# Kernel tuning notes

Measured on AMD Instinct MI355X. Metric: run time of the kernel, lower is better.

## Reference

```python
import jax, jax.numpy as jnp
import numpy as np
from jax import lax

B, H, W, CL, CC, CD, NH, NP = 8, 48, 48, 384, 384, 384, 12, 4
N = H * W
HD = CL // NH
SCALE = HD ** -0.5


def _pool_mat(n, out=7):
    # torch AdaptiveAvgPool2d bin edges: [floor(i*n/out), ceil((i+1)*n/out))
    M = np.zeros((out, n), np.float32)
    for i in range(out):
        s = (i * n) // out
        e = -(-((i + 1) * n) // out)
        M[i, s:e] = 1.0 / (e - s)
    return jnp.asarray(M)


def _resize_mat(out_n, in_n):
    # bilinear, align_corners=False (torch F.interpolate)
    M = np.zeros((out_n, in_n), np.float32)
    scale = in_n / out_n
    for o in range(out_n):
        src = (o + 0.5) * scale - 0.5
        src = min(max(src, 0.0), in_n - 1.0)
        i0 = int(np.floor(src))
        i1 = min(i0 + 1, in_n - 1)
        f = src - i0
        M[o, i0] += 1.0 - f
        M[o, i1] += f
    return jnp.asarray(M)


def _ln_c(x, g, b):
    # LayerNorm over channel dim of NCHW, eps=1e-6
    mu = jnp.mean(x, axis=1, keepdims=True)
    var = jnp.mean((x - mu) ** 2, axis=1, keepdims=True)
    xn = (x - mu) * lax.rsqrt(var + 1e-6)
    return xn * g[None, :, None, None] + b[None, :, None, None]


def _c1(x, w):
    # 1x1 conv, w: (out,in)
    return jnp.einsum('oc,bchw->bohw', w, x)


def _bilerp(feat, grid):
    # feat (G,C,Hs,Ws), grid (G,M,2) xy in [-1,1]; align_corners=False, zero padding
    G, C, Hs, Ws = feat.shape
    x = (grid[..., 0] + 1.0) * 0.5 * Ws - 0.5
    y = (grid[..., 1] + 1.0) * 0.5 * Hs - 0.5
    x0 = jnp.floor(x)
    y0 = jnp.floor(y)
    fx = x - x0
    fy = y - y0
    featf = feat.transpose(0, 2, 3, 1).reshape(G, Hs * Ws, C)
    x0i = x0.astype(jnp.int32)
    y0i = y0.astype(jnp.int32)

    def corner(ix, iy):
        valid = ((ix >= 0) & (ix < Ws) & (iy >= 0) & (iy < Hs)).astype(feat.dtype)
        flat = jnp.clip(iy, 0, Hs - 1) * Ws + jnp.clip(ix, 0, Ws - 1)
        g = jax.vmap(lambda f, i: f[i])(featf, flat)  # (G,M,C)
        return g * valid[..., None]

    v00 = corner(x0i, y0i)
    v01 = corner(x0i + 1, y0i)
    v10 = corner(x0i, y0i + 1)
    v11 = corner(x0i + 1, y0i + 1)
    w00 = ((1 - fx) * (1 - fy))[..., None]
    w01 = (fx * (1 - fy))[..., None]
    w10 = ((1 - fx) * fy)[..., None]
    w11 = (fx * fy)[..., None]
    return v00 * w00 + v01 * w01 + v10 * w10 + v11 * w11  # (G,M,C)


def _forward(local_feat, context_prior, deformable_x, W_q, W_k, W_v, W_pre, ln1_g, ln1_b,
             W_post, dw_w, dw_b, ln2_g, ln2_b, W_lo, b_lo, W_off, b_off,
             attention_biases, W_p, bn_g, bn_b, bn_mean, bn_var):
    q = _c1(local_feat, W_q)  # (B,CL,H,W)

    # context_offset_guide: 1x1 -> GELU -> adaptive pool 7x7 -> LN(C) -> 1x1 to 32 -> resize
    cg = jax.nn.gelu(_c1(context_prior, W_pre), approximate=False)
    Mh, Mw = _pool_mat(H), _pool_mat(W)
    pooled = jnp.einsum('oh,pw,bchw->bcop', Mh, Mw, cg)
    guide = _c1(_ln_c(pooled, ln1_g, ln1_b), W_post)  # (B,32,7,7)
    Uh, Uw = _resize_mat(H, 7), _resize_mat(W, 7)
    guide = jnp.einsum('Oh,Pw,bchw->bcOP', Uh, Uw, guide)  # (B,32,H,W)

    # local_offset_base: dwconv3x3 -> LN(C) -> GELU -> 1x1 to 32
    dw = lax.conv_general_dilated(local_feat, dw_w, (1, 1), [(1, 1), (1, 1)],
                                  dimension_numbers=('NCHW', 'OIHW', 'NCHW'),
                                  feature_group_count=CL) + dw_b[None, :, None, None]
    lo = jax.nn.gelu(_ln_c(dw, ln2_g, ln2_b), approximate=False)
    lo = _c1(lo, W_lo) + b_lo[None, :, None, None]  # (B,32,H,W)

    fused = jnp.concatenate([guide, lo], axis=1)  # (B,64,H,W)
    off = _c1(fused, W_off) + b_off[None, :, None, None]  # (B,NH*NP*2,H,W)
    off = off.transpose(0, 2, 3, 1).reshape(B, H, W, NH, NP, 2)
    offn = off / jnp.asarray([W, H], dtype=off.dtype)

    ry = (jnp.arange(H, dtype=off.dtype) + 0.5) / H
    rx = (jnp.arange(W, dtype=off.dtype) + 0.5) / W
    ref = jnp.stack([jnp.broadcast_to(rx[None, :], (H, W)),
                     jnp.broadcast_to(ry[:, None], (H, W))], axis=-1)  # (H,W,2) xy
    grid = (ref[None, :, :, None, None, :] + offn) * 2.0 - 1.0  # (B,H,W,NH,NP,2)

    gridh = grid.reshape(B, N, NH, NP, 2).transpose(0, 2, 1, 3, 4)  # (B,NH,N,NP,2)
    grid_r = gridh.reshape(B * NH, N * NP, 2)

    k = _c1(context_prior, W_k).reshape(B * NH, HD, H, W)
    v = _c1(deformable_x, W_v).reshape(B * NH, HD, H, W)
    k_s = _bilerp(k, grid_r).reshape(B, NH, N, NP, HD)
    v_s = _bilerp(v, grid_r).reshape(B, NH, N, NP, HD)

    qh = q.reshape(B, NH, HD, N).transpose(0, 1, 3, 2)  # (B,NH,N,HD)
    scores = jnp.einsum('bhnd,bhnpd->bhnp', qh, k_s) * SCALE

    # relative position bias: idx(p1,p2) = |dy|*W + |dx| (first-seen enumeration)
    px = jnp.clip(jnp.round((gridh[..., 0] + 1.0) * 0.5 * W - 0.5), 0, W - 1).astype(jnp.int32)
    py = jnp.clip(jnp.round((gridh[..., 1] + 1.0) * 0.5 * H - 0.5), 0, H - 1).astype(jnp.int32)
    n = jnp.arange(N, dtype=jnp.int32)
    qy = (n // W)[None, None, :, None]
    qx = (n % W)[None, None, :, None]
    bidx = jnp.abs(qy - py) * W + jnp.abs(qx - px)  # (B,NH,N,NP)
    bias = attention_biases[jnp.arange(NH)[None, :, None, None], bidx]

    attn = jax.nn.softmax(scores + bias, axis=-1)
    out = jnp.einsum('bhnp,bhnpd->bhnd', attn, v_s)  # (B,NH,N,HD)
    out = out.transpose(0, 1, 3, 2).reshape(B, CL, H, W)

    y = _c1(out, W_p)
    y = bn_g[None, :, None, None] * (y - bn_mean[None, :, None, None]) * \
        lax.rsqrt(bn_var[None, :, None, None] + 1e-5) + bn_b[None, :, None, None]
    return y


def setup_inputs():
    ks = jax.random.split(jax.random.key(0), 16)
    f32 = jnp.float32
    d = {
        'local_feat': jax.random.normal(ks[0], (B, CL, H, W), f32),
        'context_prior': jax.random.normal(ks[1], (B, CC, H, W), f32),
        'deformable_x': jax.random.normal(ks[2], (B, CD, H, W), f32),
        'W_q': jax.random.normal(ks[3], (CL, CL), f32) * 0.02,
        'W_k': jax.random.normal(ks[4], (CL, CC), f32) * 0.02,
        'W_v': jax.random.normal(ks[5], (CD, CD), f32) * 0.02,
        'W_pre': jax.random.normal(ks[6], (CC, CC), f32) * 0.02,
        'ln1_g': jnp.ones((CC,), f32),
        'ln1_b': jnp.zeros((CC,), f32),
        'W_post': jax.random.normal(ks[7], (32, CC), f32) * 0.02,
        'dw_w': jax.random.normal(ks[8], (CL, 1, 3, 3), f32) * 0.1,
        'dw_b': jnp.zeros((CL,), f32),
        'ln2_g': jnp.ones((CL,), f32),
        'ln2_b': jnp.zeros((CL,), f32),
        'W_lo': jax.random.normal(ks[9], (32, CL), f32) * 0.02,
        'b_lo': jnp.zeros((32,), f32),
        'W_off': jax.random.normal(ks[10], (NH * NP * 2, 64), f32) * 0.01,
        'b_off': jax.random.normal(ks[11], (NH * NP * 2,), f32) * 0.5,
        'attention_biases': jax.random.normal(ks[12], (NH, H * W), f32) * 0.02,
        'W_p': jax.random.normal(ks[13], (CL, CL), f32) * 0.02,
        'bn_g': jnp.ones((CL,), f32),
        'bn_b': jnp.zeros((CL,), f32),
        'bn_mean': jax.random.normal(ks[14], (CL,), f32) * 0.01,
        'bn_var': jax.random.uniform(ks[15], (CL,), f32, 0.5, 1.5),
    }
    return d


def reference(local_feat, context_prior, deformable_x, W_q, W_k, W_v, W_pre, ln1_g, ln1_b,
              W_post, dw_w, dw_b, ln2_g, ln2_b, W_lo, b_lo, W_off, b_off,
              attention_biases, W_p, bn_g, bn_b, bn_mean, bn_var):
    return _forward(local_feat, context_prior, deformable_x, W_q, W_k, W_v, W_pre, ln1_g,
                    ln1_b, W_post, dw_w, dw_b, ln2_g, ln2_b, W_lo, b_lo, W_off, b_off,
                    attention_biases, W_p, bn_g, bn_b, bn_mean, bn_var)
```

## Files before the change

### kernel.cpp

```cpp
#include <hip/hip_runtime.h>
#include <hip/hip_bf16.h>
#include <math.h>

#define B_ 8
#define H_ 48
#define W_ 48
#define N_ 2304
#define C_ 384
#define NH_ 12
#define NP_ 4
#define HD_ 32
#define SCALE_ 0.17677669529663687f

typedef unsigned short ushort;
typedef short bf16x8 __attribute__((ext_vector_type(8)));
typedef float f32x4 __attribute__((ext_vector_type(4)));

__device__ __forceinline__ float b2f(ushort u) {
    union { float f; unsigned i; } x; x.i = ((unsigned)u) << 16; return x.f;
}
__device__ __forceinline__ ushort f2b(float f) {
    __hip_bfloat16 h = __float2bfloat16(f);
    return *(ushort*)&h;
}
__device__ __forceinline__ float geluf(float x) {
    return 0.5f * x * (1.0f + erff(x * 0.70710678118654752440f));
}
__device__ __forceinline__ int iabs(int x) { return x < 0 ? -x : x; }

__device__ __forceinline__ void gl_lds16(const ushort* g, ushort* l) {
    __builtin_amdgcn_global_load_lds(
        (const __attribute__((address_space(1))) unsigned int*)g,
        (__attribute__((address_space(3))) unsigned int*)l, 16, 0, 0);
}

__global__ void probe_kernel(const void* ones_ptr, int* flag) {
    if (threadIdx.x == 0 && blockIdx.x == 0)
        *flag = (*(const unsigned*)ones_ptr == 0x3F803F80u) ? 1 : 0;
}

#define PREP_MAX 24
struct PrepTab {
    const void* src[PREP_MAX];
    void*       dst[PREP_MAX];
    int         n[PREP_MAX];
    int         tobf[PREP_MAX];
};
__global__ __launch_bounds__(256) void prep_kernel(PrepTab tab, int ne, const int* __restrict__ dflag)
{
    const int isbf = *dflag;
    const int e = blockIdx.y;
    if (e >= ne) return;
    const int n = tab.n[e];
    const void* src = tab.src[e];
    if (tab.tobf[e]) {
        ushort* dst = (ushort*)tab.dst[e];
        if (isbf) {
            const ushort* s = (const ushort*)src;
            for (int i = blockIdx.x * 256 + threadIdx.x; i < n; i += gridDim.x * 256)
                dst[i] = s[i];
        } else {
            const float* s = (const float*)src;
            for (int i = blockIdx.x * 256 + threadIdx.x; i < n; i += gridDim.x * 256)
                dst[i] = f2b(s[i]);
        }
    } else {
        float* dst = (float*)tab.dst[e];
        if (isbf) {
            const ushort* s = (const ushort*)src;
            for (int i = blockIdx.x * 256 + threadIdx.x; i < n; i += gridDim.x * 256)
                dst[i] = b2f(s[i]);
        } else {
            const float* s = (const float*)src;
            for (int i = blockIdx.x * 256 + threadIdx.x; i < n; i += gridDim.x * 256)
                dst[i] = s[i];
        }
    }
}

__global__ void dwt_prep_kernel(const float* __restrict__ WdF, float* __restrict__ WdT)
{
    int c = threadIdx.x;
#pragma unroll
    for (int u = 0; u < 9; u++) WdT[u * C_ + c] = WdF[c * 9 + u];
}

struct TPtrs { const void* src[3]; ushort* dst[3]; };
__global__ __launch_bounds__(256) void transpose3_kernel(TPtrs tp, const int* __restrict__ dflag)
{
    const int isbf = *dflag;
    const int which = blockIdx.z >> 3;
    const int b = blockIdx.z & 7;
    const int n0 = blockIdx.x * 64, c0 = blockIdx.y * 32;
    const void* in = tp.src[which];
    ushort* out = tp.dst[which];
    const int t = threadIdx.x;

    __shared__ unsigned tile[64][33];

    if (isbf) {
        {
            const int c = t >> 3, s = t & 7;
            uint4 v = *(const uint4*)((const ushort*)in + ((size_t)b * C_ + c0 + c) * N_ + n0 + s * 8);
            const int nb = s * 8;
            tile[nb + 0][c] = v.x & 0xffff; tile[nb + 1][c] = v.x >> 16;
            tile[nb + 2][c] = v.y & 0xffff; tile[nb + 3][c] = v.y >> 16;
            tile[nb + 4][c] = v.z & 0xffff; tile[nb + 5][c] = v.z >> 16;
            tile[nb + 6][c] = v.w & 0xffff; tile[nb + 7][c] = v.w >> 16;
        }
        __syncthreads();
        {
            const int n = t >> 2, s = t & 3;
            const int cb = s * 8;
            unsigned p0 = tile[n][cb + 0] | (tile[n][cb + 1] << 16);
            unsigned p1 = tile[n][cb + 2] | (tile[n][cb + 3] << 16);
            unsigned p2 = tile[n][cb + 4] | (tile[n][cb + 5] << 16);
            unsigned p3 = tile[n][cb + 6] | (tile[n][cb + 7] << 16);
            uint4 o; o.x = p0; o.y = p1; o.z = p2; o.w = p3;
            *(uint4*)(out + ((size_t)b * N_ + n0 + n) * C_ + c0 + cb) = o;
        }
    } else {
        float* tf = (float*)&tile[0][0];
        const int tx = t & 31, ty = t >> 5;
        for (int sub = 0; sub < 2; sub++) {
            int ns = n0 + sub * 32;
            __syncthreads();
#pragma unroll
            for (int u = 0; u < 4; u++) {
                int c = ty + u * 8;
                tf[c * 33 + tx] = ((const float*)in)[((size_t)b * C_ + c0 + c) * N_ + ns + tx];
            }
            __syncthreads();
#pragma unroll
            for (int u = 0; u < 4; u++) {
                int n = ty + u * 8;
                out[((size_t)b * N_ + ns + n) * C_ + c0 + tx] = f2b(tf[tx * 33 + n]);
            }
        }
    }
}

struct QKV4Ptrs { const ushort* A[4]; const ushort* Bw[4]; void* Y[4]; };
__global__ __launch_bounds__(256, 5) void gemm_qkv4_kernel(QKV4Ptrs qp)
{
    const int l = (blockIdx.x & 7) * 216 + (blockIdx.x >> 3);
    const int zc = l / 54, r2 = l % 54;
    const int which = zc >> 3, b = zc & 7;
    const int m0 = (r2 / 3) * 128;
    const int n0 = (r2 % 3) * 128;
    const ushort* Ag = qp.A[which];
    const ushort* Bg = qp.Bw[which];

    __shared__ ushort As[2][128 * 32];
    __shared__ ushort Bs[2][128 * 32];
    const int tid = threadIdx.x;
    const int lane = tid & 63, wave = tid >> 6;
    const int wr = wave >> 1, wc = wave & 1;
    const int quad = lane >> 4, l15 = lane & 15;
    const int sx = (quad ^ (l15 & 3)) * 8;

    f32x4 acc[4][4];
#pragma unroll
    for (int i = 0; i < 4; i++)
#pragma unroll
        for (int j = 0; j < 4; j++) acc[i][j] = (f32x4){0.f, 0.f, 0.f, 0.f};

    const size_t abase = (size_t)b * (size_t)N_ * C_;

    auto stage = [&](int p, int kc) {
#pragma unroll
        for (int u = 0; u < 2; u++) {
            int idx = tid + 256 * u;
            int r = idx >> 2, sl = idx & 3;
            int sg = sl ^ (r & 3);
            gl_lds16(Ag + abase + (size_t)(m0 + r) * C_ + kc + 8 * sg, &As[p][idx * 8]);
            gl_lds16(Bg + (size_t)(n0 + r) * C_ + kc + 8 * sg, &Bs[p][idx * 8]);
        }
    };

    stage(0, 0);

    const int nt = C_ / 32;
    for (int t = 0; t < nt; ++t) {
        if (t + 1 < nt) {
            stage((t + 1) & 1, (t + 1) * 32);
            asm volatile("s_waitcnt vmcnt(4)" ::: "memory");
        } else {
            asm volatile("s_waitcnt vmcnt(0)" ::: "memory");
        }
        __builtin_amdgcn_s_barrier();
        __builtin_amdgcn_sched_barrier(0);
        const int p = t & 1;
        bf16x8 af[4], bfr[4];
#pragma unroll
        for (int i = 0; i < 4; i++)
            af[i]  = *(const bf16x8*)&As[p][(wr * 64 + i * 16 + l15) * 32 + sx];
#pragma unroll
        for (int j = 0; j < 4; j++)
            bfr[j] = *(const bf16x8*)&Bs[p][(wc * 64 + j * 16 + l15) * 32 + sx];
#pragma unroll
        for (int i = 0; i < 4; i++)
#pragma unroll
            for (int j = 0; j < 4; j++)
                acc[i][j] = __builtin_amdgcn_mfma_f32_16x16x32_bf16(af[i], bfr[j], acc[i][j], 0, 0, 0);
        __builtin_amdgcn_s_barrier();
    }

    if (which < 3) {
        ushort* Yg = (ushort*)qp.Y[which];
#pragma unroll
        for (int i = 0; i < 4; i++) {
#pragma unroll
            for (int r = 0; r < 4; r++) {
                int m = m0 + wr * 64 + i * 16 + quad * 4 + r;
#pragma unroll
                for (int j = 0; j < 4; j++) {
                    int nn = n0 + wc * 64 + j * 16 + l15;
                    Yg[abase + (size_t)m * C_ + nn] = f2b(acc[i][j][r]);
                }
            }
        }
    } else {
        float* Yg = (float*)qp.Y[3];
#pragma unroll
        for (int i = 0; i < 4; i++) {
#pragma unroll
            for (int r = 0; r < 4; r++) {
                int m = m0 + wr * 64 + i * 16 + quad * 4 + r;
#pragma unroll
                for (int j = 0; j < 4; j++) {
                    int nn = n0 + wc * 64 + j * 16 + l15;
                    Yg[abase + (size_t)m * C_ + nn] = geluf(acc[i][j][r]);
                }
            }
        }
    }
}

__global__ __launch_bounds__(256) void gemm_final_kernel(
    const ushort* __restrict__ WpB, const ushort* __restrict__ AOut,
    void* __restrict__ Yg,
    const float* __restrict__ bng, const float* __restrict__ bnb,
    const float* __restrict__ bnm, const float* __restrict__ bnv,
    const int* __restrict__ dflag)
{
    const int isbf = *dflag;
    const int l = (blockIdx.x & 7) * 108 + (blockIdx.x >> 3);
    const int b = l / 108, r2 = l % 108;
    const int n0 = (r2 / 3) * 64;
    const int m0 = (r2 % 3) * 128;

    __shared__ ushort As[2][128 * 32];
    __shared__ ushort Bs[2][64 * 32];
    const int tid = threadIdx.x;
    const int lane = tid & 63, wave = tid >> 6;
    const int quad = lane >> 4, l15 = lane & 15;
    const int sx = (quad ^ (l15 & 3)) * 8;

    f32x4 acc[2][4];
#pragma unroll
    for (int i = 0; i < 2; i++)
#pragma unroll
        for (int j = 0; j < 4; j++) acc[i][j] = (f32x4){0.f, 0.f, 0.f, 0.f};

    const size_t bbase = (size_t)b * (size_t)N_ * C_;

    auto stage = [&](int p, int kc) {
#pragma unroll
        for (int u = 0; u < 2; u++) {
            int idx = tid + 256 * u;
            int r = idx >> 2, sl = idx & 3;
            int sg = sl ^ (r & 3);
            gl_lds16(WpB + (size_t)(m0 + r) * C_ + kc + 8 * sg, &As[p][idx * 8]);
        }
        {
            int r = tid >> 2, sl = tid & 3;
            int sg = sl ^ (r & 3);
            gl_lds16(AOut + bbase + (size_t)(n0 + r) * C_ + kc + 8 * sg, &Bs[p][tid * 8]);
        }
    };

    stage(0, 0);

    const int nt = C_ / 32;
    for (int t = 0; t < nt; ++t) {
        if (t + 1 < nt) {
            stage((t + 1) & 1, (t + 1) * 32);
            asm volatile("s_waitcnt vmcnt(3)" ::: "memory");
        } else {
            asm volatile("s_waitcnt vmcnt(0)" ::: "memory");
        }
        __builtin_amdgcn_s_barrier();
        __builtin_amdgcn_sched_barrier(0);
        const int p = t & 1;
        bf16x8 af[2], bfr[4];
#pragma unroll
        for (int i = 0; i < 2; i++)
            af[i]  = *(const bf16x8*)&As[p][(wave * 32 + i * 16 + l15) * 32 + sx];
#pragma unroll
        for (int j = 0; j < 4; j++)
            bfr[j] = *(const bf16x8*)&Bs[p][(j * 16 + l15) * 32 + sx];
#pragma unroll
        for (int i = 0; i < 2; i++)
#pragma unroll
            for (int j = 0; j < 4; j++)
                acc[i][j] = __builtin_amdgcn_mfma_f32_16x16x32_bf16(af[i], bfr[j], acc[i][j], 0, 0, 0);
        __builtin_amdgcn_s_barrier();
    }

    const size_t ybase = (size_t)b * (size_t)C_ * N_;
#pragma unroll
    for (int i = 0; i < 2; i++) {
#pragma unroll
        for (int r = 0; r < 4; r++) {
            int m = m0 + wave * 32 + i * 16 + quad * 4 + r;
            float sc = bng[m] * rsqrtf(bnv[m] + 1e-5f);
            float sh = bnb[m] - sc * bnm[m];
#pragma unroll
            for (int j = 0; j < 4; j++) {
                int nn = n0 + j * 16 + l15;
                float v = sc * acc[i][j][r] + sh;
                size_t yi = ybase + (size_t)m * N_ + nn;
                if (isbf) ((ushort*)Yg)[yi] = f2b(v);
                else ((float*)Yg)[yi] = v;
            }
        }
    }
}

__global__ __launch_bounds__(384) void pool_ln_guide_kernel(
    const float* __restrict__ CG, const float* __restrict__ g, const float* __restrict__ bt,
    const ushort* __restrict__ WpostB, float* __restrict__ G7)
{
    const int cell = blockIdx.x % 49, b = blockIdx.x / 49;
    const int i = cell / 7, j = cell % 7, c = threadIdx.x;
    const int sh = (i * H_) / 7, eh = ((i + 1) * H_ + 6) / 7;
    const int sw = (j * W_) / 7, ew = ((j + 1) * W_ + 6) / 7;
    float s = 0.f;
    for (int h = sh; h < eh; h++)
        for (int w = sw; w < ew; w++)
            s += CG[((size_t)b * N_ + h * W_ + w) * C_ + c];
    s *= 1.0f / (float)((eh - sh) * (ew - sw));

    float rs = s, rq = s * s;
#pragma unroll
    for (int m = 1; m <= 32; m <<= 1) {
        rs += __shfl_xor(rs, m);
        rq += __shfl_xor(rq, m);
    }
    __shared__ float ss[6], sq[6], buf[C_];
    __shared__ float psum[12][33];
    int wid = threadIdx.x >> 6;
    if ((threadIdx.x & 63) == 0) { ss[wid] = rs; sq[wid] = rq; }
    __syncthreads();
    if (threadIdx.x == 0) {
        float ts = 0.f, tq = 0.f;
        for (int k = 0; k < 6; k++) { ts += ss[k]; tq += sq[k]; }
        ss[0] = ts; sq[0] = tq;
    }
    __syncthreads();
    float mu = ss[0] / (float)C_;
    float var = sq[0] / (float)C_ - mu * mu;
    float inv = rsqrtf(var + 1e-6f);
    buf[c] = (s - mu) * inv * g[c] + bt[c];
    __syncthreads();

    const int oc = threadIdx.x & 31, seg = threadIdx.x >> 5;
    const uint4* wp = (const uint4*)(WpostB + oc * C_ + seg * 32);
    float part = 0.f;
#pragma unroll
    for (int u = 0; u < 4; u++) {
        uint4 v = wp[u];
        const float* bb = &buf[seg * 32 + u * 8];
        part += b2f((ushort)(v.x & 0xffff)) * bb[0] + b2f((ushort)(v.x >> 16)) * bb[1];
        part += b2f((ushort)(v.y & 0xffff)) * bb[2] + b2f((ushort)(v.y >> 16)) * bb[3];
        part += b2f((ushort)(v.z & 0xffff)) * bb[4] + b2f((ushort)(v.z >> 16)) * bb[5];
        part += b2f((ushort)(v.w & 0xffff)) * bb[6] + b2f((ushort)(v.w >> 16)) * bb[7];
    }
    psum[seg][oc] = part;
    __syncthreads();
    if (threadIdx.x < 32) {
        float acc = 0.f;
#pragma unroll
        for (int k = 0; k < 12; k++) acc += psum[k][threadIdx.x];
        G7[((size_t)b * 49 + cell) * 32 + threadIdx.x] = acc;
    }
}

__global__ __launch_bounds__(384) void wcomb_prep_kernel(
    const ushort* __restrict__ WoffB, const ushort* __restrict__ WloB,
    const float* __restrict__ bloF, const float* __restrict__ boffF,
    ushort* __restrict__ Bext, float* __restrict__ biasp)
{
    const int co = blockIdx.x;
    const int c = threadIdx.x;
    float acc = 0.f;
#pragma unroll 8
    for (int j = 0; j < 32; j++)
        acc += b2f(WoffB[co * 64 + 32 + j]) * b2f(WloB[j * 384 + c]);
    ushort hi = f2b(acc);
    float r = acc - b2f(hi);
    ushort lo = f2b(r);
    Bext[co * 1152 + c] = hi;
    Bext[co * 1152 + 384 + c] = lo;
    Bext[co * 1152 + 768 + c] = hi;
    if (c == 0) {
        float bp = boffF[co];
        for (int j = 0; j < 32; j++)
            bp += b2f(WoffB[co * 64 + 32 + j]) * bloF[j];
        biasp[co] = bp;
    }
}

__global__ void og7_prep_kernel(
    const ushort* __restrict__ WoffB, const float* __restrict__ G7, float* __restrict__ OG7)
{
    const int bc = blockIdx.x;
    const int co = threadIdx.x;
    if (co >= 96) return;
    const float* g = G7 + (size_t)bc * 32;
    float acc = 0.f;
#pragma unroll 8
    for (int c = 0; c < 32; c++)
        acc += b2f(WoffB[co * 64 + c]) * g[c];
    OG7[(size_t)bc * 96 + co] = acc;
}

__global__ __launch_bounds__(512) void dw_ln_gelu_kernel(
    const ushort* __restrict__ LF, const float* __restrict__ WdT, const float* __restrict__ BdF,
    const float* __restrict__ g, const float* __restrict__ bt,
    ushort* __restrict__ AHI, ushort* __restrict__ ALO)
{
    const int wave = threadIdx.x >> 6, lane = threadIdx.x & 63;
    const int m = blockIdx.x * 8 + wave;
    const int b = m / N_, n = m % N_;
    const int h = n / W_, w = n % W_;
    const bool act = lane < 48;
    const int c0 = lane * 8;

    float acc[8];
#pragma unroll
    for (int j = 0; j < 8; j++) acc[j] = 0.f;
    if (act) {
        f32x4 b0 = *(const f32x4*)(BdF + c0);
        f32x4 b1 = *(const f32x4*)(BdF + c0 + 4);
#pragma unroll
        for (int j = 0; j < 4; j++) { acc[j] = b0[j]; acc[4 + j] = b1[j]; }
    }

#pragma unroll
    for (int u = 0; u < 9; u++) {
        const int ky = u / 3, kx = u % 3;
        const int y = h + ky - 1, x = w + kx - 1;
        if (act && y >= 0 && y < H_ && x >= 0 && x < W_) {
            uint4 v = *(const uint4*)(LF + ((size_t)b * N_ + y * W_ + x) * C_ + c0);
            f32x4 wa = *(const f32x4*)(WdT + u * C_ + c0);
            f32x4 wb = *(const f32x4*)(WdT + u * C_ + c0 + 4);
            acc[0] += wa[0] * b2f((ushort)(v.x & 0xffff));
            acc[1] += wa[1] * b2f((ushort)(v.x >> 16));
            acc[2] += wa[2] * b2f((ushort)(v.y & 0xffff));
            acc[3] += wa[3] * b2f((ushort)(v.y >> 16));
            acc[4] += wb[0] * b2f((ushort)(v.z & 0xffff));
            acc[5] += wb[1] * b2f((ushort)(v.z >> 16));
            acc[6] += wb[2] * b2f((ushort)(v.w & 0xffff));
            acc[7] += wb[3] * b2f((ushort)(v.w >> 16));
        }
    }

    float rs = 0.f, rq = 0.f;
#pragma unroll
    for (int j = 0; j < 8; j++) { rs += acc[j]; rq += acc[j] * acc[j]; }
#pragma unroll
    for (int s = 1; s <= 32; s <<= 1) {
        rs += __shfl_xor(rs, s);
        rq += __shfl_xor(rq, s);
    }
    float mu = rs / (float)C_;
    float var = rq / (float)C_ - mu * mu;
    float inv = rsqrtf(var + 1e-6f);

    if (act) {
        f32x4 g0 = *(const f32x4*)(g + c0);
        f32x4 g1 = *(const f32x4*)(g + c0 + 4);
        f32x4 t0 = *(const f32x4*)(bt + c0);
        f32x4 t1 = *(const f32x4*)(bt + c0 + 4);
        float v[8];
#pragma unroll
        for (int j = 0; j < 4; j++) {
            v[j]     = geluf((acc[j]     - mu) * inv * g0[j] + t0[j]);
            v[4 + j] = geluf((acc[4 + j] - mu) * inv * g1[j] + t1[j]);
        }
        uint4 hi, lo;
        ushort hs[8], ls[8];
#pragma unroll
        for (int j = 0; j < 8; j++) {
            hs[j] = f2b(v[j]);
            ls[j] = f2b(v[j] - b2f(hs[j]));
        }
        hi.x = (unsigned)hs[0] | ((unsigned)hs[1] << 16);
        hi.y = (unsigned)hs[2] | ((unsigned)hs[3] << 16);
        hi.z = (unsigned)hs[4] | ((unsigned)hs[5] << 16);
        hi.w = (unsigned)hs[6] | ((unsigned)hs[7] << 16);
        lo.x = (unsigned)ls[0] | ((unsigned)ls[1] << 16);
        lo.y = (unsigned)ls[2] | ((unsigned)ls[3] << 16);
        lo.z = (unsigned)ls[4] | ((unsigned)ls[5] << 16);
        lo.w = (unsigned)ls[6] | ((unsigned)ls[7] << 16);
        size_t idx = (size_t)m * C_ + c0;
        *(uint4*)(AHI + idx) = hi;
        *(uint4*)(ALO + idx) = lo;
    }
}

__global__ __launch_bounds__(256) void off_gemm_kernel(
    const ushort* __restrict__ AHI, const ushort* __restrict__ ALO,
    const ushort* __restrict__ Bext, float* __restrict__ OFFP)
{
    __shared__ ushort As[4][128 * 32];
    __shared__ ushort Bs[4][128 * 32];
    const int tid = threadIdx.x;
    const int m0 = blockIdx.x * 128;
    const int seg = blockIdx.y;
    const ushort* Ag = (seg < 2) ? AHI : ALO;
    const int bcol0 = seg * 384;
    const int lane = tid & 63, wave = tid >> 6;
    const int wr = wave >> 1, wc = wave & 1;
    const int quad = lane >> 4, l15 = lane & 15;
    const int sx = (quad ^ (l15 & 3)) * 8;

    f32x4 acc[4][3];
#pragma unroll
    for (int i = 0; i < 4; i++)
#pragma unroll
        for (int j = 0; j < 3; j++) acc[i][j] = (f32x4){0.f, 0.f, 0.f, 0.f};

    auto stage = [&](int p, int kc) {
#pragma unroll
        for (int u = 0; u < 2; u++) {
            int idx = tid + 256 * u;
            int r = idx >> 2, sl = idx & 3;
            int sg = sl ^ (r & 3);
            int rb = r < 96 ? r : 95;
            gl_lds16(Ag + (size_t)(m0 + r) * 384 + kc + 8 * sg, &As[p][idx * 8]);
            gl_lds16(Bext + (size_t)rb * 1152 + bcol0 + kc + 8 * sg, &Bs[p][idx * 8]);
        }
    };

    stage(0, 0);
    stage(1, 32);
    stage(2, 64);

    const int nt = 12;
    for (int t = 0; t < nt; ++t) {
        if (t + 2 < nt)      asm volatile("s_waitcnt vmcnt(8)" ::: "memory");
        else if (t + 1 < nt) asm volatile("s_waitcnt vmcnt(4)" ::: "memory");
        else                 asm volatile("s_waitcnt vmcnt(0)" ::: "memory");
        __builtin_amdgcn_s_barrier();
        __builtin_amdgcn_sched_barrier(0);
        if (t + 3 < nt) stage((t + 3) & 3, (t + 3) * 32);
        const int p = t & 3;
        bf16x8 af[4], bfr[3];
#pragma unroll
        for (int i = 0; i < 4; i++)
            af[i]  = *(const bf16x8*)&As[p][(wr * 64 + i * 16 + l15) * 32 + sx];
#pragma unroll
        for (int j = 0; j < 3; j++)
            bfr[j] = *(const bf16x8*)&Bs[p][(wc * 48 + j * 16 + l15) * 32 + sx];
#pragma unroll
        for (int i = 0; i < 4; i++)
#pragma unroll
            for (int j = 0; j < 3; j++)
                acc[i][j] = __builtin_amdgcn_mfma_f32_16x16x32_bf16(af[i], bfr[j], acc[i][j], 0, 0, 0);
    }

    float* out = OFFP + (size_t)seg * ((size_t)B_ * N_ * 96);
#pragma unroll
    for (int i = 0; i < 4; i++) {
#pragma unroll
        for (int r = 0; r < 4; r++) {
            int m = m0 + wr * 64 + i * 16 + quad * 4 + r;
#pragma unroll
            for (int j = 0; j < 3; j++) {
                int co = wc * 48 + j * 16 + l15;
                out[(size_t)m * 96 + co] = acc[i][j][r];
            }
        }
    }
}

__global__ __launch_bounds__(384) void attn_kernel(
    const ushort* __restrict__ Q, const ushort* __restrict__ K, const ushort* __restrict__ V,
    const float* __restrict__ OFFP, const float* __restrict__ biasp,
    const float* __restrict__ OG7,
    const float* __restrict__ ABf, ushort* __restrict__ OUT)
{
    const int pairi = blockIdx.x;
    const int b = pairi / (N_ / 2);
    const int n0 = (pairi % (N_ / 2)) * 2;
    const int tid = threadIdx.x;

    __shared__ int   cidxS[96][4];
    __shared__ float cwS[96][4];
    __shared__ float biasS[96];

    if (tid < 96) {
        const int pos = tid / 48, idx = tid % 48;
        const int n = n0 + pos;
        const int h = n / W_, w = n % W_;
        const int nh = idx >> 2, p = idx & 3;
        const int co = nh * 8 + 2 * p;

        const float fs = 7.0f / 48.0f;
        float sy = fminf(fmaxf(((float)h + 0.5f) * fs - 0.5f, 0.f), 6.f);
        float sx = fminf(fmaxf(((float)w + 0.5f) * fs - 0.5f, 0.f), 6.f);
        int gy0 = (int)floorf(sy), gx0 = (int)floorf(sx);
        int gy1 = min(gy0 + 1, 6), gx1 = min(gx0 + 1, 6);
        float gfy = sy - (float)gy0, gfx = sx - (float)gx0;
        float bw00 = (1.f - gfy) * (1.f - gfx), bw01 = (1.f - gfy) * gfx;
        float bw10 = gfy * (1.f - gfx), bw11 = gfy * gfx;
        const float* ogb = OG7 + (size_t)b * 49 * 96;
        int c00 = (gy0 * 7 + gx0) * 96, c01 = (gy0 * 7 + gx1) * 96;
        int c10 = (gy1 * 7 + gx0) * 96, c11 = (gy1 * 7 + gx1) * 96;
        const size_t MS = (size_t)B_ * N_ * 96;
        const size_t mrow = ((size_t)b * N_ + n) * 96;

        float ox = OFFP[mrow + co] + OFFP[MS + mrow + co] + OFFP[2 * MS + mrow + co]
                 + biasp[co]
                 + bw00 * ogb[c00 + co] + bw01 * ogb[c01 + co]
                 + bw10 * ogb[c10 + co] + bw11 * ogb[c11 + co];
        float oy = OFFP[mrow + co + 1] + OFFP[MS + mrow + co + 1] + OFFP[2 * MS + mrow + co + 1]
                 + biasp[co + 1]
                 + bw00 * ogb[c00 + co + 1] + bw01 * ogb[c01 + co + 1]
                 + bw10 * ogb[c10 + co + 1] + bw11 * ogb[c11 + co + 1];

        float x = (float)w + ox;
        float y = (float)h + oy;

        int px = (int)fminf(fmaxf(rintf(x), 0.f), (float)(W_ - 1));
        int py = (int)fminf(fmaxf(rintf(y), 0.f), (float)(H_ - 1));
        biasS[tid] = ABf[(size_t)nh * N_ + iabs(h - py) * W_ + iabs(w - px)];

        float x0f = floorf(x), y0f = floorf(y);
        float fx = x - x0f, fy = y - y0f;
        int x0 = (int)x0f, y0 = (int)y0f;
#pragma unroll
        for (int cc = 0; cc < 4; cc++) {
            int dx = cc & 1, dy = cc >> 1;
            int ix = x0 + dx, iy = y0 + dy;
            bool valid = (ix >= 0) && (ix < W_) && (iy >= 0) && (iy < H_);
            int ixc = min(max(ix, 0), W_ - 1), iyc = min(max(iy, 0), H_ - 1);
            cidxS[tid][cc] = iyc * W_ + ixc;
            float wx = dx ? fx : (1.f - fx);
            float wy = dy ? fy : (1.f - fy);
            cwS[tid][cc] = valid ? wx * wy : 0.f;
        }
    }
    __syncthreads();

    const int pos = tid / 192, r = tid % 192;
    const int nh = r >> 4, dd = r & 15;
    const int n = n0 + pos;
    const size_t row = ((size_t)b * N_ + n) * C_ + nh * HD_ + dd * 2;
    unsigned qu = *(const unsigned*)(Q + row);
    const float q0 = b2f((ushort)(qu & 0xffff));
    const float q1 = b2f((ushort)(qu >> 16));
    const size_t kvbase = (size_t)b * N_ * C_ + nh * HD_ + dd * 2;
    const int s0 = pos * 48 + nh * 4;

    int   ci[NP_][4];
    float cw[NP_][4];
#pragma unroll
    for (int p = 0; p < NP_; p++)
#pragma unroll
        for (int cc = 0; cc < 4; cc++) {
            ci[p][cc] = cidxS[s0 + p][cc];
            cw[p][cc] = cwS[s0 + p][cc];
        }

    float sc[NP_];
#pragma unroll
    for (int p = 0; p < NP_; p++) {
        float ks0 = 0.f, ks1 = 0.f;
#pragma unroll
        for (int cc = 0; cc < 4; cc++) {
            unsigned kv = *(const unsigned*)(K + kvbase + (size_t)ci[p][cc] * C_);
            ks0 += cw[p][cc] * b2f((ushort)(kv & 0xffff));
            ks1 += cw[p][cc] * b2f((ushort)(kv >> 16));
        }
        float dot = q0 * ks0 + q1 * ks1;
#pragma unroll
        for (int m = 1; m <= 8; m <<= 1) dot += __shfl_xor(dot, m);
        sc[p] = dot * SCALE_ + biasS[s0 + p];
    }

    float m = fmaxf(fmaxf(sc[0], sc[1]), fmaxf(sc[2], sc[3]));
    float e[NP_], esum = 0.f;
#pragma unroll
    for (int p = 0; p < NP_; p++) { e[p] = __expf(sc[p] - m); esum += e[p]; }
    float inv = 1.0f / esum;

    float o0 = 0.f, o1 = 0.f;
#pragma unroll
    for (int p = 0; p < NP_; p++) {
        float vs0 = 0.f, vs1 = 0.f;
#pragma unroll
        for (int cc = 0; cc < 4; cc++) {
            unsigned vv = *(const unsigned*)(V + kvbase + (size_t)ci[p][cc] * C_);
            vs0 += cw[p][cc] * b2f((ushort)(vv & 0xffff));
            vs1 += cw[p][cc] * b2f((ushort)(vv >> 16));
        }
        float ep = e[p] * inv;
        o0 += ep * vs0;
        o1 += ep * vs1;
    }
    unsigned ou = (unsigned)f2b(o0) | ((unsigned)f2b(o1) << 16);
    *(unsigned*)(OUT + row) = ou;
}

extern "C" void kernel_launch(void* const* d_in, const int* in_sizes, int n_in,
                              void* d_out, int out_size, void* d_ws, size_t ws_size,
                              hipStream_t stream)
{
    const void* local_feat    = d_in[0];
    const void* context_prior = d_in[1];
    const void* deformable_x  = d_in[2];

    const size_t BIGE = (size_t)B_ * N_ * C_;

    char* wsb = (char*)d_ws;
    auto carve = [&](size_t bytes) { char* p = wsb; wsb += (bytes + 255) & ~(size_t)255; return p; };
    int*    flag = (int*)carve(256);
    ushort* T1   = (ushort*)carve(BIGE * 2);
    ushort* T2   = (ushort*)carve(BIGE * 2);
    ushort* T3   = (ushort*)carve(BIGE * 2);
    ushort* Qb   = (ushort*)carve(BIGE * 2);
    ushort* Kb   = (ushort*)carve(BIGE * 2);
    ushort* Vb   = (ushort*)carve(BIGE * 2);
    ushort* AHI  = (ushort*)carve(BIGE * 2);
    ushort* ALO  = (ushort*)carve(BIGE * 2);
    float*  CGR  = (float*)carve(BIGE * 4);
    float*  OFFB = (float*)carve((size_t)B_ * N_ * 96 * 4 * 3);
    float*  G7   = (float*)carve((size_t)B_ * 49 * 32 * 4);
    ushort* WqB   = (ushort*)carve(147456 * 2);
    ushort* WkB   = (ushort*)carve(147456 * 2);
    ushort* WvB   = (ushort*)carve(147456 * 2);
    ushort* WpreB = (ushort*)carve(147456 * 2);
    ushort* WpB   = (ushort*)carve(147456 * 2);
    ushort* WpostB= (ushort*)carve(12288 * 2);
    ushort* WloB  = (ushort*)carve(12288 * 2);
    ushort* WoffB = (ushort*)carve(6144 * 2);
    ushort* Bext  = (ushort*)carve(96 * 1152 * 2);
    float*  biasp = (float*)carve(96 * 4);
    float*  OG7   = (float*)carve((size_t)B_ * 49 * 96 * 4);
    float*  dwwF  = (float*)carve(3456 * 4);
    float*  dwwT  = (float*)carve(3456 * 4);
    float*  ABf   = (float*)carve(27648 * 4);
    float*  bloF  = (float*)carve(32 * 4);
    float*  boffF = (float*)carve(96 * 4);
    float*  dwbF  = (float*)carve(384 * 4);
    float*  ln1gF = (float*)carve(384 * 4);
    float*  ln1bF = (float*)carve(384 * 4);
    float*  ln2gF = (float*)carve(384 * 4);
    float*  ln2bF = (float*)carve(384 * 4);
    float*  bngF  = (float*)carve(384 * 4);
    float*  bnbF  = (float*)carve(384 * 4);
    float*  bnmF  = (float*)carve(384 * 4);
    float*  bnvF  = (float*)carve(384 * 4);
    ushort* AOut = (ushort*)CGR + BIGE;

    probe_kernel<<<1, 64, 0, stream>>>(d_in[7] , flag);

    PrepTab tab;
    int ne = 0;
    auto add = [&](const void* s, void* d, int n, int tb) {
        tab.src[ne] = s; tab.dst[ne] = d; tab.n[ne] = n; tab.tobf[ne] = tb; ne++;
    };
    add(d_in[3],  WqB,   147456, 1);
    add(d_in[4],  WkB,   147456, 1);
    add(d_in[5],  WvB,   147456, 1);
    add(d_in[6],  WpreB, 147456, 1);
    add(d_in[19], WpB,   147456, 1);
    add(d_in[9],  WpostB, 12288, 1);
    add(d_in[14], WloB,   12288, 1);
    add(d_in[16], WoffB,   6144, 1);
    add(d_in[10], dwwF,    3456, 0);
    add(d_in[18], ABf,    27648, 0);
    add(d_in[15], bloF,      32, 0);
    add(d_in[17], boffF,     96, 0);
    add(d_in[11], dwbF,     384, 0);
    add(d_in[7],  ln1gF,    384, 0);
    add(d_in[8],  ln1bF,    384, 0);
    add(d_in[12], ln2gF,    384, 0);
    add(d_in[13], ln2bF,    384, 0);
    add(d_in[20], bngF,     384, 0);
    add(d_in[21], bnbF,     384, 0);
    add(d_in[22], bnmF,     384, 0);
    add(d_in[23], bnvF,     384, 0);
    prep_kernel<<<dim3(64, ne), 256, 0, stream>>>(tab, ne, flag);
    dwt_prep_kernel<<<1, 384, 0, stream>>>(dwwF, dwwT);

    dim3 blk256(256);
    dim3 t3grid(N_ / 64, C_ / 32, 3 * B_);
    dim3 offgrid((B_ * N_) / 128, 3);

    TPtrs tp;
    tp.src[0] = local_feat;    tp.dst[0] = T1;
    tp.src[1] = context_prior; tp.dst[1] = T2;
    tp.src[2] = deformable_x;  tp.dst[2] = T3;
    transpose3_kernel<<<t3grid, blk256, 0, stream>>>(tp, flag);

    wcomb_prep_kernel<<<96, 384, 0, stream>>>(WoffB, WloB, bloF, boffF, Bext, biasp);

    dw_ln_gelu_kernel<<<(B_ * N_) / 8, 512, 0, stream>>>(T1, dwwT, dwbF, ln2gF, ln2bF, AHI, ALO);

    off_gemm_kernel<<<offgrid, blk256, 0, stream>>>(AHI, ALO, Bext, OFFB);

    QKV4Ptrs qp;
    qp.A[0] = T1; qp.Bw[0] = WqB;   qp.Y[0] = Qb;
    qp.A[1] = T2; qp.Bw[1] = WkB;   qp.Y[1] = Kb;
    qp.A[2] = T3; qp.Bw[2] = WvB;   qp.Y[2] = Vb;
    qp.A[3] = T2; qp.Bw[3] = WpreB; qp.Y[3] = CGR;
    gemm_qkv4_kernel<<<1728, blk256, 0, stream>>>(qp);

    pool_ln_guide_kernel<<<B_ * 49, 384, 0, stream>>>(CGR, ln1gF, ln1bF, WpostB, G7);
    og7_prep_kernel<<<B_ * 49, 96, 0, stream>>>(WoffB, G7, OG7);

    attn_kernel<<<(B_ * N_) / 2, 384, 0, stream>>>(Qb, Kb, Vb, OFFB, biasp, OG7, ABf, AOut);

    gemm_final_kernel<<<864, blk256, 0, stream>>>(
        WpB, AOut, d_out, bngF, bnbF, bnmF, bnvF, flag);
}
```

Before: 346.4 us.

## Merge offset GEMM into QKV GEMM launch and fold og7 prep into pool kernel

The separate offset-projection GEMM is folded into the QKV/pre GEMM as extra leading blocks of one 2160-block launch. The og7 projection is computed at the end of pool_ln_guide_kernel through shared memory, so two kernel launches and the G7 round trip through global memory go away. In exchange, the offset GEMM drops from a 4-deep to a 2-deep staging pipeline. Both GEMMs also lose their XOR LDS swizzle and the XCD block remapping, which risks LDS bank conflicts and worse cache locality.

```diff
diff --git a/kernel.cpp b/kernel.cpp
--- a/kernel.cpp
+++ b/kernel.cpp
@@ -141,96 +141,162 @@
 }
 
 struct QKV4Ptrs { const ushort* A[4]; const ushort* Bw[4]; void* Y[4]; };
-__global__ __launch_bounds__(256, 5) void gemm_qkv4_kernel(QKV4Ptrs qp)
-{
-    const int l = (blockIdx.x & 7) * 216 + (blockIdx.x >> 3);
-    const int zc = l / 54, r2 = l % 54;
-    const int which = zc >> 3, b = zc & 7;
-    const int m0 = (r2 / 3) * 128;
-    const int n0 = (r2 % 3) * 128;
-    const ushort* Ag = qp.A[which];
-    const ushort* Bg = qp.Bw[which];
-
+__global__ __launch_bounds__(256, 5) void mega_gemm_kernel(
+    QKV4Ptrs qp,
+    const ushort* __restrict__ AHI, const ushort* __restrict__ ALO,
+    const ushort* __restrict__ Bext, float* __restrict__ OFFP)
+{
     __shared__ ushort As[2][128 * 32];
     __shared__ ushort Bs[2][128 * 32];
     const int tid = threadIdx.x;
     const int lane = tid & 63, wave = tid >> 6;
     const int wr = wave >> 1, wc = wave & 1;
     const int quad = lane >> 4, l15 = lane & 15;
-    const int sx = (quad ^ (l15 & 3)) * 8;
-
-    f32x4 acc[4][4];
-#pragma unroll
-    for (int i = 0; i < 4; i++)
-#pragma unroll
-        for (int j = 0; j < 4; j++) acc[i][j] = (f32x4){0.f, 0.f, 0.f, 0.f};
-
-    const size_t abase = (size_t)b * (size_t)N_ * C_;
-
-    auto stage = [&](int p, int kc) {
-#pragma unroll
-        for (int u = 0; u < 2; u++) {
-            int idx = tid + 256 * u;
-            int r = idx >> 2, sl = idx & 3;
-            int sg = sl ^ (r & 3);
-            gl_lds16(Ag + abase + (size_t)(m0 + r) * C_ + kc + 8 * sg, &As[p][idx * 8]);
-            gl_lds16(Bg + (size_t)(n0 + r) * C_ + kc + 8 * sg, &Bs[p][idx * 8]);
-        }
-    };
-
-    stage(0, 0);
-
-    const int nt = C_ / 32;
-    for (int t = 0; t < nt; ++t) {
-        if (t + 1 < nt) {
-            stage((t + 1) & 1, (t + 1) * 32);
-            asm volatile("s_waitcnt vmcnt(4)" ::: "memory");
-        } else {
-            asm volatile("s_waitcnt vmcnt(0)" ::: "memory");
-        }
-        __builtin_amdgcn_s_barrier();
-        __builtin_amdgcn_sched_barrier(0);
-        const int p = t & 1;
-        bf16x8 af[4], bfr[4];
+    const int bid = blockIdx.x;
+
+    if (bid < 432) {
+        const int seg = bid % 3;
+        const int m0 = (bid / 3) * 128;
+        const ushort* Ag = (seg < 2) ? AHI : ALO;
+        const int bcol0 = seg * 384;
+
+        f32x4 acc[4][3];
 #pragma unroll
         for (int i = 0; i < 4; i++)
-            af[i]  = *(const bf16x8*)&As[p][(wr * 64 + i * 16 + l15) * 32 + sx];
-#pragma unroll
-        for (int j = 0; j < 4; j++)
-            bfr[j] = *(const bf16x8*)&Bs[p][(wc * 64 + j * 16 + l15) * 32 + sx];
-#pragma unroll
-        for (int i = 0; i < 4; i++)
-#pragma unroll
-            for (int j = 0; j < 4; j++)
-                acc[i][j] = __builtin_amdgcn_mfma_f32_16x16x32_bf16(af[i], bfr[j], acc[i][j], 0, 0, 0);
-        __builtin_amdgcn_s_barrier();
-    }
-
-    if (which < 3) {
-        ushort* Yg = (ushort*)qp.Y[which];
+#pragma unroll
+            for (int j = 0; j < 3; j++) acc[i][j] = (f32x4){0.f, 0.f, 0.f, 0.f};
+
+        auto stage = [&](int p, int kc) {
+#pragma unroll
+            for (int u = 0; u < 2; u++) {
+                int idx = tid + 256 * u;
+                int r = idx >> 2, s = idx & 3;
+                int rb = r < 96 ? r : 95;
+                gl_lds16(Ag + (size_t)(m0 + r) * 384 + kc + 8 * s, &As[p][idx * 8]);
+                gl_lds16(Bext + (size_t)rb * 1152 + bcol0 + kc + 8 * s, &Bs[p][idx * 8]);
+            }
+        };
+
+        stage(0, 0);
+        const int nt = 12;
+        for (int t = 0; t < nt; ++t) {
+            if (t + 1 < nt) {
+                stage((t + 1) & 1, (t + 1) * 32);
+                asm volatile("s_waitcnt vmcnt(4)" ::: "memory");
+            } else {
+                asm volatile("s_waitcnt vmcnt(0)" ::: "memory");
+            }
+            __builtin_amdgcn_s_barrier();
+            __builtin_amdgcn_sched_barrier(0);
+            const int p = t & 1;
+            bf16x8 af[4], bfr[3];
+#pragma unroll
+            for (int i = 0; i < 4; i++)
+                af[i]  = *(const bf16x8*)&As[p][(wr * 64 + i * 16 + l15) * 32 + quad * 8];
+#pragma unroll
+            for (int j = 0; j < 3; j++)
+                bfr[j] = *(const bf16x8*)&Bs[p][(wc * 48 + j * 16 + l15) * 32 + quad * 8];
+#pragma unroll
+            for (int i = 0; i < 4; i++)
+#pragma unroll
+                for (int j = 0; j < 3; j++)
+                    acc[i][j] = __builtin_amdgcn_mfma_f32_16x16x32_bf16(af[i], bfr[j], acc[i][j], 0, 0, 0);
+            __builtin_amdgcn_s_barrier();
+        }
+
+        float* out = OFFP + (size_t)seg * ((size_t)B_ * N_ * 96);
 #pragma unroll
         for (int i = 0; i < 4; i++) {
 #pragma unroll
             for (int r = 0; r < 4; r++) {
                 int m = m0 + wr * 64 + i * 16 + quad * 4 + r;
 #pragma unroll
-                for (int j = 0; j < 4; j++) {
-                    int nn = n0 + wc * 64 + j * 16 + l15;
-                    Yg[abase + (size_t)m * C_ + nn] = f2b(acc[i][j][r]);
+                for (int j = 0; j < 3; j++) {
+                    int co = wc * 48 + j * 16 + l15;
+                    out[(size_t)m * 96 + co] = acc[i][j][r];
                 }
             }
         }
     } else {
-        float* Yg = (float*)qp.Y[3];
-#pragma unroll
-        for (int i = 0; i < 4; i++) {
-#pragma unroll
-            for (int r = 0; r < 4; r++) {
-                int m = m0 + wr * 64 + i * 16 + quad * 4 + r;
-#pragma unroll
-                for (int j = 0; j < 4; j++) {
-                    int nn = n0 + wc * 64 + j * 16 + l15;
-                    Yg[abase + (size_t)m * C_ + nn] = geluf(acc[i][j][r]);
+        const int q = bid - 432;
+        const int zc = q / 54, r2 = q % 54;
+        const int which = zc >> 3, b = zc & 7;
+        const int m0 = (r2 / 3) * 128;
+        const int n0 = (r2 % 3) * 128;
+        const ushort* Ag = qp.A[which];
+        const ushort* Bg = qp.Bw[which];
+
+        f32x4 acc[4][4];
+#pragma unroll
+        for (int i = 0; i < 4; i++)
+#pragma unroll
+            for (int j = 0; j < 4; j++) acc[i][j] = (f32x4){0.f, 0.f, 0.f, 0.f};
+
+        const size_t abase = (size_t)b * (size_t)N_ * C_;
+
+        auto stage = [&](int p, int kc) {
+#pragma unroll
+            for (int u = 0; u < 2; u++) {
+                int idx = tid + 256 * u;
+                int r = idx >> 2, s = idx & 3;
+                gl_lds16(Ag + abase + (size_t)(m0 + r) * C_ + kc + 8 * s, &As[p][idx * 8]);
+                gl_lds16(Bg + (size_t)(n0 + r) * C_ + kc + 8 * s, &Bs[p][idx * 8]);
+            }
+        };
+
+        stage(0, 0);
+        const int nt = C_ / 32;
+        for (int t = 0; t < nt; ++t) {
+            if (t + 1 < nt) {
+                stage((t + 1) & 1, (t + 1) * 32);
+                asm volatile("s_waitcnt vmcnt(4)" ::: "memory");
+            } else {
+                asm volatile("s_waitcnt vmcnt(0)" ::: "memory");
+            }
+            __builtin_amdgcn_s_barrier();
+            __builtin_amdgcn_sched_barrier(0);
+            const int p = t & 1;
+            bf16x8 af[4], bfr[4];
+#pragma unroll
+            for (int i = 0; i < 4; i++)
+                af[i]  = *(const bf16x8*)&As[p][(wr * 64 + i * 16 + l15) * 32 + quad * 8];
+#pragma unroll
+            for (int j = 0; j < 4; j++)
+                bfr[j] = *(const bf16x8*)&Bs[p][(wc * 64 + j * 16 + l15) * 32 + quad * 8];
+#pragma unroll
+            for (int i = 0; i < 4; i++)
+#pragma unroll
+                for (int j = 0; j < 4; j++)
+                    acc[i][j] = __builtin_amdgcn_mfma_f32_16x16x32_bf16(af[i], bfr[j], acc[i][j], 0, 0, 0);
+            __builtin_amdgcn_s_barrier();
+        }
+
+        if (which < 3) {
+            ushort* Yg = (ushort*)qp.Y[which];
+#pragma unroll
+            for (int i = 0; i < 4; i++) {
+#pragma unroll
+                for (int r = 0; r < 4; r++) {
+                    int m = m0 + wr * 64 + i * 16 + quad * 4 + r;
+#pragma unroll
+                    for (int j = 0; j < 4; j++) {
+                        int nn = n0 + wc * 64 + j * 16 + l15;
+                        Yg[abase + (size_t)m * C_ + nn] = f2b(acc[i][j][r]);
+                    }
+                }
+            }
+        } else {
+            float* Yg = (float*)qp.Y[3];
+#pragma unroll
+            for (int i = 0; i < 4; i++) {
+#pragma unroll
+                for (int r = 0; r < 4; r++) {
+                    int m = m0 + wr * 64 + i * 16 + quad * 4 + r;
+#pragma unroll
+                    for (int j = 0; j < 4; j++) {
+                        int nn = n0 + wc * 64 + j * 16 + l15;
+                        Yg[abase + (size_t)m * C_ + nn] = geluf(acc[i][j][r]);
+                    }
                 }
             }
         }
@@ -330,7 +396,8 @@
 
 __global__ __launch_bounds__(384) void pool_ln_guide_kernel(
     const float* __restrict__ CG, const float* __restrict__ g, const float* __restrict__ bt,
-    const ushort* __restrict__ WpostB, float* __restrict__ G7)
+    const ushort* __restrict__ WpostB, const ushort* __restrict__ WoffB,
+    float* __restrict__ OG7)
 {
     const int cell = blockIdx.x % 49, b = blockIdx.x / 49;
     const int i = cell / 7, j = cell % 7, c = threadIdx.x;
@@ -350,6 +417,7 @@
     }
     __shared__ float ss[6], sq[6], buf[C_];
     __shared__ float psum[12][33];
+    __shared__ float g7s[32];
     int wid = threadIdx.x >> 6;
     if ((threadIdx.x & 63) == 0) { ss[wid] = rs; sq[wid] = rq; }
     __syncthreads();
@@ -383,7 +451,16 @@
         float acc = 0.f;
 #pragma unroll
         for (int k = 0; k < 12; k++) acc += psum[k][threadIdx.x];
-        G7[((size_t)b * 49 + cell) * 32 + threadIdx.x] = acc;
+        g7s[threadIdx.x] = acc;
+    }
+    __syncthreads();
+    if (threadIdx.x < 96) {
+        const int co = threadIdx.x;
+        float acc = 0.f;
+#pragma unroll 8
+        for (int k = 0; k < 32; k++)
+            acc += b2f(WoffB[co * 64 + k]) * g7s[k];
+        OG7[(size_t)blockIdx.x * 96 + co] = acc;
     }
 }
 
@@ -412,20 +489,6 @@
     }
 }
 
-__global__ void og7_prep_kernel(
-    const ushort* __restrict__ WoffB, const float* __restrict__ G7, float* __restrict__ OG7)
-{
-    const int bc = blockIdx.x;
-    const int co = threadIdx.x;
-    if (co >= 96) return;
-    const float* g = G7 + (size_t)bc * 32;
-    float acc = 0.f;
-#pragma unroll 8
-    for (int c = 0; c < 32; c++)
-        acc += b2f(WoffB[co * 64 + c]) * g[c];
-    OG7[(size_t)bc * 96 + co] = acc;
-}
-
 __global__ __launch_bounds__(512) void dw_ln_gelu_kernel(
     const ushort* __restrict__ LF, const float* __restrict__ WdT, const float* __restrict__ BdF,
     const float* __restrict__ g, const float* __restrict__ bt,
@@ -508,82 +571,6 @@
         size_t idx = (size_t)m * C_ + c0;
         *(uint4*)(AHI + idx) = hi;
         *(uint4*)(ALO + idx) = lo;
-    }
-}
-
-__global__ __launch_bounds__(256) void off_gemm_kernel(
-    const ushort* __restrict__ AHI, const ushort* __restrict__ ALO,
-    const ushort* __restrict__ Bext, float* __restrict__ OFFP)
-{
-    __shared__ ushort As[4][128 * 32];
-    __shared__ ushort Bs[4][128 * 32];
-    const int tid = threadIdx.x;
-    const int m0 = blockIdx.x * 128;
-    const int seg = blockIdx.y;
-    const ushort* Ag = (seg < 2) ? AHI : ALO;
-    const int bcol0 = seg * 384;
-    const int lane = tid & 63, wave = tid >> 6;
-    const int wr = wave >> 1, wc = wave & 1;
-    const int quad = lane >> 4, l15 = lane & 15;
-    const int sx = (quad ^ (l15 & 3)) * 8;
-
-    f32x4 acc[4][3];
-#pragma unroll
-    for (int i = 0; i < 4; i++)
-#pragma unroll
-        for (int j = 0; j < 3; j++) acc[i][j] = (f32x4){0.f, 0.f, 0.f, 0.f};
-
-    auto stage = [&](int p, int kc) {
-#pragma unroll
-        for (int u = 0; u < 2; u++) {
-            int idx = tid + 256 * u;
-            int r = idx >> 2, sl = idx & 3;
-            int sg = sl ^ (r & 3);
-            int rb = r < 96 ? r : 95;
-            gl_lds16(Ag + (size_t)(m0 + r) * 384 + kc + 8 * sg, &As[p][idx * 8]);
-            gl_lds16(Bext + (size_t)rb * 1152 + bcol0 + kc + 8 * sg, &Bs[p][idx * 8]);
-        }
-    };
-
-    stage(0, 0);
-    stage(1, 32);
-    stage(2, 64);
-
-    const int nt = 12;
-    for (int t = 0; t < nt; ++t) {
-        if (t + 2 < nt)      asm volatile("s_waitcnt vmcnt(8)" ::: "memory");
-        else if (t + 1 < nt) asm volatile("s_waitcnt vmcnt(4)" ::: "memory");
-        else                 asm volatile("s_waitcnt vmcnt(0)" ::: "memory");
-        __builtin_amdgcn_s_barrier();
-        __builtin_amdgcn_sched_barrier(0);
-        if (t + 3 < nt) stage((t + 3) & 3, (t + 3) * 32);
-        const int p = t & 3;
-        bf16x8 af[4], bfr[3];
-#pragma unroll
-        for (int i = 0; i < 4; i++)
-            af[i]  = *(const bf16x8*)&As[p][(wr * 64 + i * 16 + l15) * 32 + sx];
-#pragma unroll
-        for (int j = 0; j < 3; j++)
-            bfr[j] = *(const bf16x8*)&Bs[p][(wc * 48 + j * 16 + l15) * 32 + sx];
-#pragma unroll
-        for (int i = 0; i < 4; i++)
-#pragma unroll
-            for (int j = 0; j < 3; j++)
-                acc[i][j] = __builtin_amdgcn_mfma_f32_16x16x32_bf16(af[i], bfr[j], acc[i][j], 0, 0, 0);
-    }
-
-    float* out = OFFP + (size_t)seg * ((size_t)B_ * N_ * 96);
-#pragma unroll
-    for (int i = 0; i < 4; i++) {
-#pragma unroll
-        for (int r = 0; r < 4; r++) {
-            int m = m0 + wr * 64 + i * 16 + quad * 4 + r;
-#pragma unroll
-            for (int j = 0; j < 3; j++) {
-                int co = wc * 48 + j * 16 + l15;
-                out[(size_t)m * 96 + co] = acc[i][j][r];
-            }
-        }
     }
 }
 
@@ -766,6 +753,7 @@
     float*  bnmF  = (float*)carve(384 * 4);
     float*  bnvF  = (float*)carve(384 * 4);
     ushort* AOut = (ushort*)CGR + BIGE;
+    (void)G7;
 
     probe_kernel<<<1, 64, 0, stream>>>(d_in[7] , flag);
 
@@ -800,7 +788,6 @@
 
     dim3 blk256(256);
     dim3 t3grid(N_ / 64, C_ / 32, 3 * B_);
-    dim3 offgrid((B_ * N_) / 128, 3);
 
     TPtrs tp;
     tp.src[0] = local_feat;    tp.dst[0] = T1;
@@ -812,17 +799,14 @@
 
     dw_ln_gelu_kernel<<<(B_ * N_) / 8, 512, 0, stream>>>(T1, dwwT, dwbF, ln2gF, ln2bF, AHI, ALO);
 
-    off_gemm_kernel<<<offgrid, blk256, 0, stream>>>(AHI, ALO, Bext, OFFB);
-
     QKV4Ptrs qp;
     qp.A[0] = T1; qp.Bw[0] = WqB;   qp.Y[0] = Qb;
     qp.A[1] = T2; qp.Bw[1] = WkB;   qp.Y[1] = Kb;
     qp.A[2] = T3; qp.Bw[2] = WvB;   qp.Y[2] = Vb;
     qp.A[3] = T2; qp.Bw[3] = WpreB; qp.Y[3] = CGR;
-    gemm_qkv4_kernel<<<1728, blk256, 0, stream>>>(qp);
-
-    pool_ln_guide_kernel<<<B_ * 49, 384, 0, stream>>>(CGR, ln1gF, ln1bF, WpostB, G7);
-    og7_prep_kernel<<<B_ * 49, 96, 0, stream>>>(WoffB, G7, OG7);
+    mega_gemm_kernel<<<2160, blk256, 0, stream>>>(qp, AHI, ALO, Bext, OFFB);
+
+    pool_ln_guide_kernel<<<B_ * 49, 384, 0, stream>>>(CGR, ln1gF, ln1bF, WpostB, WoffB, OG7);
 
     attn_kernel<<<(B_ * N_) / 2, 384, 0, stream>>>(Qb, Kb, Vb, OFFB, biasp, OG7, ABf, AOut);
 
```

Measured after the change: 354.2 us. 1.02x slower.
